# Performance work log

Hardware: AMD Instinct MI355X
Metric: run time of the kernel (lower is better)

The kernel has to match this reference:

```python
import jax, jax.numpy as jnp
import numpy as np

B, S, D = 4, 2048, 1024
H = 16
HD = D // H  # 64

def setup_inputs() -> dict:
    key = jax.random.key(0)
    ks = jax.random.split(key, 7)
    s = 0.02
    return {
        "x": jax.random.normal(ks[0], (B, S, D), dtype=jnp.float32),
        "Wq": jax.random.normal(ks[1], (D, D), dtype=jnp.float32) * s,
        "bq": jax.random.normal(ks[2], (D,), dtype=jnp.float32) * s,
        "Wk": jax.random.normal(ks[3], (D, D), dtype=jnp.float32) * s,
        "bk": jax.random.normal(ks[4], (D,), dtype=jnp.float32) * s,
        "Wv": jax.random.normal(ks[5], (D, D), dtype=jnp.float32) * s,
        "bv": jax.random.normal(ks[6], (D,), dtype=jnp.float32) * s,
    }

def reference(x, Wq, bq, Wk, bk, Wv, bv):
    bs, seq, _ = x.shape
    q = (x @ Wq.T + bq).reshape(bs, seq, H, HD).transpose(0, 2, 1, 3)  # [b,h,s,d]
    k = (x @ Wk.T + bk).reshape(bs, seq, H, HD).transpose(0, 2, 1, 3)
    v = (x @ Wv.T + bv).reshape(bs, seq, H, HD).transpose(0, 2, 1, 3)
    scores = jnp.einsum('bhqd,bhkd->bhqk', q, k) / jnp.sqrt(jnp.float32(HD))
    probs = jax.nn.softmax(scores, axis=-1)  # dropout p=0 -> identity
    att = jnp.einsum('bhqk,bhkd->bhqd', probs, v)
    return att.transpose(0, 2, 1, 3).reshape(bs, seq, H * HD)
```

## Files before the change

kernel.cpp:

```cpp
#include <hip/hip_runtime.h>

typedef __bf16 bf16x8 __attribute__((ext_vector_type(8)));
typedef float f32x4 __attribute__((ext_vector_type(4)));
typedef float f32x16 __attribute__((ext_vector_type(16)));

#define BATCH 4
#define SEQ   2048
#define DIM   1024
#define NH    16
#define HD    64
#define ECF   0.18033688f

__device__ __forceinline__ unsigned short f2bf(float f) {
  union { float f; unsigned u; } v; v.f = f;
  unsigned u = v.u;
  u += 0x7FFF + ((u >> 16) & 1);
  return (unsigned short)(u >> 16);
}

__device__ __forceinline__ void g2lds16(const unsigned short* g, unsigned short* l) {
  __builtin_amdgcn_global_load_lds(
      (const __attribute__((address_space(1))) unsigned int*)g,
      (__attribute__((address_space(3))) unsigned int*)l, 16, 0, 0);
}

__device__ __forceinline__ unsigned packbf(float a, float b) {
  __bf16 lo = (__bf16)a, hi = (__bf16)b;
  unsigned short ul = __builtin_bit_cast(unsigned short, lo);
  unsigned short uh = __builtin_bit_cast(unsigned short, hi);
  return (unsigned)ul | ((unsigned)uh << 16);
}

__global__ __launch_bounds__(256) void cast_all_kernel(
    const float* __restrict__ x,  const float* __restrict__ Wq,
    const float* __restrict__ Wk, const float* __restrict__ Wv,
    unsigned short* __restrict__ xb,  unsigned short* __restrict__ wqb,
    unsigned short* __restrict__ wkb, unsigned short* __restrict__ wvb) {
  const int XG = (BATCH * SEQ * DIM) / 8;
  const int WG = (DIM * DIM) / 8;
  int i = blockIdx.x * 256 + threadIdx.x;
  const float* in; unsigned short* out; float sc = 1.0f; int off;
  if (i < XG)               { in = x;  out = xb;  off = i; }
  else if (i < XG + WG)     { in = Wq; out = wqb; off = i - XG; sc = ECF; }
  else if (i < XG + 2 * WG) { in = Wk; out = wkb; off = i - XG - WG; }
  else                      { in = Wv; out = wvb; off = i - XG - 2 * WG; }
  const float4* p = (const float4*)in + (size_t)off * 2;
  float4 a = p[0], b = p[1];
  unsigned short r[8];
  r[0] = f2bf(a.x * sc); r[1] = f2bf(a.y * sc); r[2] = f2bf(a.z * sc); r[3] = f2bf(a.w * sc);
  r[4] = f2bf(b.x * sc); r[5] = f2bf(b.y * sc); r[6] = f2bf(b.z * sc); r[7] = f2bf(b.w * sc);
  *(uint4*)&out[(size_t)off * 8] = *(uint4*)r;
}

__global__ __launch_bounds__(256) void gemm_qkv(
    const unsigned short* __restrict__ A,
    const unsigned short* __restrict__ Wqp, const unsigned short* __restrict__ Wkp,
    const unsigned short* __restrict__ Wvp,
    const float* __restrict__ bqp, const float* __restrict__ bkp,
    const float* __restrict__ bvp,
    unsigned short* __restrict__ oq, unsigned short* __restrict__ ok,
    unsigned short* __restrict__ ov) {
  __shared__ unsigned short As[128 * 32];
  __shared__ unsigned short Bs[128 * 32];
  const int z = blockIdx.z;
  const unsigned short* W = (z == 0) ? Wqp : (z == 1) ? Wkp : Wvp;
  const float* bias        = (z == 0) ? bqp : (z == 1) ? bkp : bvp;
  unsigned short* outp     = (z == 0) ? oq  : (z == 1) ? ok  : ov;
  const float bsc          = (z == 0) ? ECF : 1.0f;
  const int mode = (z == 2) ? 1 : 0;

  const int tid  = threadIdx.x;
  const int wave = tid >> 6;
  const int lane = tid & 63;
  const int lm   = lane & 15;
  const int qd   = lane >> 4;
  const int m0 = blockIdx.x * 128;
  const int n0 = blockIdx.y * 128;
  const int wm = (wave >> 1) * 64;
  const int wn = (wave & 1) * 64;

  const f32x4 zero = {0.f, 0.f, 0.f, 0.f};
  f32x4 acc[4][4];
#pragma unroll
  for (int i = 0; i < 4; ++i)
#pragma unroll
    for (int j = 0; j < 4; ++j) acc[i][j] = zero;

  const int srow = tid >> 2;
  const int scol = (((tid & 3) ^ ((tid >> 3) & 3))) * 8;
  const int cs   = (qd ^ ((lm >> 1) & 3)) * 8;

  for (int kt = 0; kt < DIM; kt += 32) {
    __syncthreads();
    g2lds16(&A[(size_t)(m0 + srow) * DIM + kt + scol],       &As[(size_t)tid * 8]);
    g2lds16(&A[(size_t)(m0 + 64 + srow) * DIM + kt + scol],  &As[2048 + (size_t)tid * 8]);
    g2lds16(&W[(size_t)(n0 + srow) * DIM + kt + scol],       &Bs[(size_t)tid * 8]);
    g2lds16(&W[(size_t)(n0 + 64 + srow) * DIM + kt + scol],  &Bs[2048 + (size_t)tid * 8]);
    __syncthreads();

    bf16x8 af[4], bfr[4];
#pragma unroll
    for (int i = 0; i < 4; ++i) af[i]  = *(const bf16x8*)&As[(wm + i * 16 + lm) * 32 + cs];
#pragma unroll
    for (int j = 0; j < 4; ++j) bfr[j] = *(const bf16x8*)&Bs[(wn + j * 16 + lm) * 32 + cs];
#pragma unroll
    for (int i = 0; i < 4; ++i)
#pragma unroll
      for (int j = 0; j < 4; ++j)
        acc[i][j] = __builtin_amdgcn_mfma_f32_16x16x32_bf16(af[i], bfr[j], acc[i][j], 0, 0, 0);
  }

#pragma unroll
  for (int j = 0; j < 4; ++j) {
    int col = n0 + wn + j * 16 + lm;
    float bb = bias[col] * bsc;
    int h = col >> 6, hd = col & 63;
#pragma unroll
    for (int i = 0; i < 4; ++i) {
      int rowb = m0 + wm + i * 16 + qd * 4;
      int b = rowb >> 11, s = rowb & 2047;
      if (mode == 0) {
#pragma unroll
        for (int r = 0; r < 4; ++r) {
          float v = acc[i][j][r] + bb;
          outp[((size_t)(b * NH + h) * SEQ + (s + r)) * HD + hd] = f2bf(v);
        }
      } else {
        unsigned short pk[4];
#pragma unroll
        for (int r = 0; r < 4; ++r) pk[r] = f2bf(acc[i][j][r] + bb);
        size_t idx = ((size_t)(b * NH + h) * HD + hd) * SEQ + s;
        *(uint2*)&outp[idx] = *(uint2*)pk;
      }
    }
  }
}

__global__ __launch_bounds__(256, 2) void flash_kernel(
    const unsigned short* __restrict__ Qp, const unsigned short* __restrict__ Kp,
    const unsigned short* __restrict__ Vp, float* __restrict__ out) {
  __shared__ __align__(16) unsigned short Ks[2][64 * 64];
  __shared__ __align__(16) unsigned short Vs[2][64 * 64];
  __shared__ float Ls[4][2][32];

  const int tid  = threadIdx.x;
  const int w    = tid >> 6;
  const int wpar = w & 1;
  const int lane = tid & 63;
  const int l31  = lane & 31;
  const int hi   = lane >> 5;
  const int bh   = blockIdx.y;
  const int wq0  = blockIdx.x * 256 + w * 64;

  const unsigned short* Qb = Qp + (size_t)bh * (SEQ * HD);
  const unsigned short* Kb = Kp + (size_t)bh * (SEQ * HD);
  const unsigned short* Vb = Vp + (size_t)bh * (HD * SEQ);

  bf16x8 qf[2][4];
#pragma unroll
  for (int qb = 0; qb < 2; ++qb)
#pragma unroll
    for (int db = 0; db < 4; ++db)
      qf[qb][db] = *(const bf16x8*)&Qb[(size_t)(wq0 + qb * 32 + l31) * HD + db * 16 + hi * 8];

  f32x16 o[2][2];
#pragma unroll
  for (int qb = 0; qb < 2; ++qb)
#pragma unroll
    for (int jn = 0; jn < 2; ++jn)
#pragma unroll
      for (int r = 0; r < 16; ++r) o[qb][jn][r] = 0.f;
  float psum[2] = {0.f, 0.f};

  const int c0 = tid, c1 = tid + 256;
  const int kr0 = c0 >> 3, kp0 = ((c0 & 7) ^ (kr0 & 7)) * 8;
  const int kr1 = c1 >> 3, kp1 = ((c1 & 7) ^ (kr1 & 7)) * 8;
  const int r7 = l31 & 7;

  auto STAGE = [&](int buf, int k0) {
    g2lds16(&Kb[(size_t)(k0 + kr0) * HD + kp0], &Ks[buf][c0 * 8]);
    g2lds16(&Kb[(size_t)(k0 + kr1) * HD + kp1], &Ks[buf][c1 * 8]);
    g2lds16(&Vb[(size_t)kr0 * SEQ + k0 + kp0],  &Vs[buf][c0 * 8]);
    g2lds16(&Vb[(size_t)kr1 * SEQ + k0 + kp1],  &Vs[buf][c1 * 8]);
  };

  STAGE(0, 0);
  int cur = 0;
  for (int kt = 0; kt < SEQ / 64; ++kt) {
    __syncthreads();
    if (kt + 1 < SEQ / 64) STAGE(cur ^ 1, (kt + 1) * 64);

    const unsigned short* Kc = &Ks[cur][0];
    const unsigned short* Vc = &Vs[cur][0];

    const int kbA = wpar;
    const int kbB = wpar ^ 1;

    f32x16 sA0 = {0,0,0,0,0,0,0,0,0,0,0,0,0,0,0,0};
    f32x16 sA1 = {0,0,0,0,0,0,0,0,0,0,0,0,0,0,0,0};
    f32x16 sB0 = {0,0,0,0,0,0,0,0,0,0,0,0,0,0,0,0};
    f32x16 sB1 = {0,0,0,0,0,0,0,0,0,0,0,0,0,0,0,0};
    __builtin_amdgcn_s_setprio(1);
#pragma unroll
    for (int db = 0; db < 4; ++db) {
      int ch = (db * 2 + hi) ^ r7;
      bf16x8 kf = *(const bf16x8*)&Kc[((kbA * 32 + l31) * 8 + ch) * 8];
      sA0 = __builtin_amdgcn_mfma_f32_32x32x16_bf16(kf, qf[0][db], sA0, 0, 0, 0);
      sA1 = __builtin_amdgcn_mfma_f32_32x32x16_bf16(kf, qf[1][db], sA1, 0, 0, 0);
    }
    __builtin_amdgcn_s_setprio(0);
#pragma unroll
    for (int db = 0; db < 4; ++db) {
      int ch = (db * 2 + hi) ^ r7;
      bf16x8 kf = *(const bf16x8*)&Kc[((kbB * 32 + l31) * 8 + ch) * 8];
      sB0 = __builtin_amdgcn_mfma_f32_32x32x16_bf16(kf, qf[0][db], sB0, 0, 0, 0);
      sB1 = __builtin_amdgcn_mfma_f32_32x32x16_bf16(kf, qf[1][db], sB1, 0, 0, 0);
    }

    bf16x8 paA[2][2], paB[2][2];
#define EXPPACK(SQ0, SQ1, PA) do {                                            \
    _Pragma("unroll")                                                         \
    for (int qb = 0; qb < 2; ++qb) {                                          \
      const f32x16 s = qb ? (SQ1) : (SQ0);                                    \
      float p[16];                                                            \
      _Pragma("unroll")                                                       \
      for (int r = 0; r < 16; ++r) p[r] = __builtin_amdgcn_exp2f(s[r]);       \
      psum[qb] += ((p[0] + p[1]) + (p[2] + p[3])) + ((p[4] + p[5]) + (p[6] + p[7]))  \
                + ((p[8] + p[9]) + (p[10] + p[11])) + ((p[12] + p[13]) + (p[14] + p[15])); \
      unsigned w01 = packbf(p[0],  p[1]),  w23 = packbf(p[2],  p[3]);         \
      unsigned w45 = packbf(p[4],  p[5]),  w67 = packbf(p[6],  p[7]);         \
      unsigned w89 = packbf(p[8],  p[9]),  wab = packbf(p[10], p[11]);        \
      unsigned wcd = packbf(p[12], p[13]), wef = packbf(p[14], p[15]);        \
      asm volatile("v_permlane32_swap_b32 %0, %1" : "+v"(w01), "+v"(w45));    \
      asm volatile("v_permlane32_swap_b32 %0, %1" : "+v"(w23), "+v"(w67));    \
      asm volatile("v_permlane32_swap_b32 %0, %1" : "+v"(w89), "+v"(wcd));    \
      asm volatile("v_permlane32_swap_b32 %0, %1" : "+v"(wab), "+v"(wef));    \
      union { unsigned u[4]; bf16x8 v; } flo, fhi;                            \
      flo.u[0] = w01; flo.u[1] = w23; flo.u[2] = w45; flo.u[3] = w67;         \
      fhi.u[0] = w89; fhi.u[1] = wab; fhi.u[2] = wcd; fhi.u[3] = wef;         \
      (PA)[qb][0] = flo.v;                                                    \
      (PA)[qb][1] = fhi.v;                                                    \
    }                                                                         \
  } while (0)

#define PVHALF(KB, PA) do {                                                   \
    _Pragma("unroll")                                                         \
    for (int ksl = 0; ksl < 2; ++ksl) {                                       \
      int ks = (KB) * 2 + ksl;                                                \
      _Pragma("unroll")                                                       \
      for (int jn = 0; jn < 2; ++jn) {                                        \
        int ch = (ks * 2 + hi) ^ r7;                                          \
        bf16x8 vf = *(const bf16x8*)&Vc[((jn * 32 + l31) * 8 + ch) * 8];      \
        o[0][jn] = __builtin_amdgcn_mfma_f32_32x32x16_bf16((PA)[0][ksl], vf, o[0][jn], 0, 0, 0); \
        o[1][jn] = __builtin_amdgcn_mfma_f32_32x32x16_bf16((PA)[1][ksl], vf, o[1][jn], 0, 0, 0); \
      }                                                                       \
    }                                                                         \
  } while (0)

    EXPPACK(sA0, sA1, paA);
    __builtin_amdgcn_s_setprio(1);
    PVHALF(kbA, paA);
    __builtin_amdgcn_s_setprio(0);
    EXPPACK(sB0, sB1, paB);
    __builtin_amdgcn_s_setprio(1);
    PVHALF(kbB, paB);
    __builtin_amdgcn_s_setprio(0);

#undef EXPPACK
#undef PVHALF
    cur ^= 1;
  }

#pragma unroll
  for (int qb = 0; qb < 2; ++qb) {
    float l = psum[qb] + __shfl_xor(psum[qb], 32);
    if (hi == 0) Ls[w][qb][l31] = 1.0f / l;
  }
  asm volatile("s_waitcnt lgkmcnt(0)" ::: "memory");

  const int b = bh >> 4, hh = bh & 15;
#pragma unroll
  for (int qb = 0; qb < 2; ++qb)
#pragma unroll
    for (int r = 0; r < 16; ++r) {
      int crow = (r & 3) + 8 * (r >> 2) + 4 * hi;
      float inv = Ls[w][qb][crow];
      int qrow = wq0 + qb * 32 + crow;
      float* po = &out[(size_t)(b * SEQ + qrow) * DIM + hh * HD + l31];
      po[0]  = o[qb][0][r] * inv;
      po[32] = o[qb][1][r] * inv;
    }
}

extern "C" void kernel_launch(void* const* d_in, const int* in_sizes, int n_in,
                              void* d_out, int out_size, void* d_ws, size_t ws_size,
                              hipStream_t stream) {
  const float* x  = (const float*)d_in[0];
  const float* Wq = (const float*)d_in[1];
  const float* bq = (const float*)d_in[2];
  const float* Wk = (const float*)d_in[3];
  const float* bk = (const float*)d_in[4];
  const float* Wv = (const float*)d_in[5];
  const float* bv = (const float*)d_in[6];
  float* out = (float*)d_out;

  unsigned short* ws = (unsigned short*)d_ws;
  const size_t XE = (size_t)BATCH * SEQ * DIM;
  const size_t WE = (size_t)DIM * DIM;
  unsigned short* xb  = ws;
  unsigned short* wqb = xb + XE;
  unsigned short* wkb = wqb + WE;
  unsigned short* wvb = wkb + WE;
  unsigned short* qb  = wvb + WE;
  unsigned short* kb  = qb + XE;
  unsigned short* vb  = kb + XE;

  const int total_groups = (int)(XE / 8 + 3 * (WE / 8));
  cast_all_kernel<<<total_groups / 256, 256, 0, stream>>>(
      x, Wq, Wk, Wv, xb, wqb, wkb, wvb);

  dim3 gg(64, 8, 3);
  gemm_qkv<<<gg, 256, 0, stream>>>(xb, wqb, wkb, wvb, bq, bk, bv, qb, kb, vb);

  dim3 fg(SEQ / 256, BATCH * NH);
  flash_kernel<<<fg, 256, 0, stream>>>(qb, kb, vb, out);
}
```

Baseline: 251.0 us.

## Triple-buffer K/V tiles and interleave staged loads with MFMA phases via barriers

Replaces the double-buffered K/V pipeline with a three-slot ring that prefetches two tiles ahead. Global-to-LDS copies are split into four pieces, each issued inside a different compute phase (QK^T halves, PV halves). Explicit s_barrier calls and vmcnt waits keep the waves in lockstep. The intent is to hide load latency and spread memory traffic across the loop. It also drops the per-wave-parity ordering of K halves, so all waves now read the same LDS rows at the same time. The costs are more LDS per block, which could limit occupancy at two blocks per CU, and many more barriers per iteration.

Measured after the change: 247.8 us. No clear change (-1.2%).

```diff
diff --git a/kernel.cpp b/kernel.cpp
--- a/kernel.cpp
+++ b/kernel.cpp
@@ -139,13 +139,12 @@
 __global__ __launch_bounds__(256, 2) void flash_kernel(
     const unsigned short* __restrict__ Qp, const unsigned short* __restrict__ Kp,
     const unsigned short* __restrict__ Vp, float* __restrict__ out) {
-  __shared__ __align__(16) unsigned short Ks[2][64 * 64];
-  __shared__ __align__(16) unsigned short Vs[2][64 * 64];
+  __shared__ __align__(16) unsigned short Ks[3][64 * 64];
+  __shared__ __align__(16) unsigned short Vs[3][64 * 64];
   __shared__ float Ls[4][2][32];
 
   const int tid  = threadIdx.x;
   const int w    = tid >> 6;
-  const int wpar = w & 1;
   const int lane = tid & 63;
   const int l31  = lane & 31;
   const int hi   = lane >> 5;
@@ -177,47 +176,12 @@
   const int kr1 = c1 >> 3, kp1 = ((c1 & 7) ^ (kr1 & 7)) * 8;
   const int r7 = l31 & 7;
 
-  auto STAGE = [&](int buf, int k0) {
-    g2lds16(&Kb[(size_t)(k0 + kr0) * HD + kp0], &Ks[buf][c0 * 8]);
-    g2lds16(&Kb[(size_t)(k0 + kr1) * HD + kp1], &Ks[buf][c1 * 8]);
-    g2lds16(&Vb[(size_t)kr0 * SEQ + k0 + kp0],  &Vs[buf][c0 * 8]);
-    g2lds16(&Vb[(size_t)kr1 * SEQ + k0 + kp1],  &Vs[buf][c1 * 8]);
-  };
-
-  STAGE(0, 0);
-  int cur = 0;
-  for (int kt = 0; kt < SEQ / 64; ++kt) {
-    __syncthreads();
-    if (kt + 1 < SEQ / 64) STAGE(cur ^ 1, (kt + 1) * 64);
-
-    const unsigned short* Kc = &Ks[cur][0];
-    const unsigned short* Vc = &Vs[cur][0];
-
-    const int kbA = wpar;
-    const int kbB = wpar ^ 1;
-
-    f32x16 sA0 = {0,0,0,0,0,0,0,0,0,0,0,0,0,0,0,0};
-    f32x16 sA1 = {0,0,0,0,0,0,0,0,0,0,0,0,0,0,0,0};
-    f32x16 sB0 = {0,0,0,0,0,0,0,0,0,0,0,0,0,0,0,0};
-    f32x16 sB1 = {0,0,0,0,0,0,0,0,0,0,0,0,0,0,0,0};
-    __builtin_amdgcn_s_setprio(1);
-#pragma unroll
-    for (int db = 0; db < 4; ++db) {
-      int ch = (db * 2 + hi) ^ r7;
-      bf16x8 kf = *(const bf16x8*)&Kc[((kbA * 32 + l31) * 8 + ch) * 8];
-      sA0 = __builtin_amdgcn_mfma_f32_32x32x16_bf16(kf, qf[0][db], sA0, 0, 0, 0);
-      sA1 = __builtin_amdgcn_mfma_f32_32x32x16_bf16(kf, qf[1][db], sA1, 0, 0, 0);
-    }
-    __builtin_amdgcn_s_setprio(0);
-#pragma unroll
-    for (int db = 0; db < 4; ++db) {
-      int ch = (db * 2 + hi) ^ r7;
-      bf16x8 kf = *(const bf16x8*)&Kc[((kbB * 32 + l31) * 8 + ch) * 8];
-      sB0 = __builtin_amdgcn_mfma_f32_32x32x16_bf16(kf, qf[0][db], sB0, 0, 0, 0);
-      sB1 = __builtin_amdgcn_mfma_f32_32x32x16_bf16(kf, qf[1][db], sB1, 0, 0, 0);
-    }
-
-    bf16x8 paA[2][2], paB[2][2];
+#define SK0(buf, k0) g2lds16(&Kb[(size_t)((k0) + kr0) * HD + kp0], &Ks[buf][c0 * 8])
+#define SK1(buf, k0) g2lds16(&Kb[(size_t)((k0) + kr1) * HD + kp1], &Ks[buf][c1 * 8])
+#define SV0(buf, k0) g2lds16(&Vb[(size_t)kr0 * SEQ + (k0) + kp0],  &Vs[buf][c0 * 8])
+#define SV1(buf, k0) g2lds16(&Vb[(size_t)kr1 * SEQ + (k0) + kp1],  &Vs[buf][c1 * 8])
+#define BAR() asm volatile("s_barrier" ::: "memory")
+
 #define EXPPACK(SQ0, SQ1, PA) do {                                            \
     _Pragma("unroll")                                                         \
     for (int qb = 0; qb < 2; ++qb) {                                          \
@@ -243,32 +207,103 @@
     }                                                                         \
   } while (0)
 
-#define PVHALF(KB, PA) do {                                                   \
-    _Pragma("unroll")                                                         \
-    for (int ksl = 0; ksl < 2; ++ksl) {                                       \
-      int ks = (KB) * 2 + ksl;                                                \
-      _Pragma("unroll")                                                       \
-      for (int jn = 0; jn < 2; ++jn) {                                        \
-        int ch = (ks * 2 + hi) ^ r7;                                          \
-        bf16x8 vf = *(const bf16x8*)&Vc[((jn * 32 + l31) * 8 + ch) * 8];      \
-        o[0][jn] = __builtin_amdgcn_mfma_f32_32x32x16_bf16((PA)[0][ksl], vf, o[0][jn], 0, 0, 0); \
-        o[1][jn] = __builtin_amdgcn_mfma_f32_32x32x16_bf16((PA)[1][ksl], vf, o[1][jn], 0, 0, 0); \
-      }                                                                       \
-    }                                                                         \
-  } while (0)
-
-    EXPPACK(sA0, sA1, paA);
-    __builtin_amdgcn_s_setprio(1);
-    PVHALF(kbA, paA);
-    __builtin_amdgcn_s_setprio(0);
-    EXPPACK(sB0, sB1, paB);
-    __builtin_amdgcn_s_setprio(1);
-    PVHALF(kbB, paB);
-    __builtin_amdgcn_s_setprio(0);
-
-#undef EXPPACK
-#undef PVHALF
-    cur ^= 1;
+  SK0(0, 0);  SK1(0, 0);  SV0(0, 0);  SV1(0, 0);
+  SK0(1, 64); SK1(1, 64); SV0(1, 64); SV1(1, 64);
+  asm volatile("s_waitcnt vmcnt(4)" ::: "memory");
+  BAR();
+
+  for (int kt = 0; kt < 32; ++kt) {
+    const int cur = kt % 3;
+    const int nb  = (kt + 2) % 3;
+    const bool st = (kt + 2) < 32;
+    const int k2  = (kt + 2) * 64;
+    const unsigned short* Kc = &Ks[cur][0];
+    const unsigned short* Vc = &Vs[cur][0];
+
+    f32x16 sA0 = {0,0,0,0,0,0,0,0,0,0,0,0,0,0,0,0};
+    f32x16 sA1 = {0,0,0,0,0,0,0,0,0,0,0,0,0,0,0,0};
+    {
+      bf16x8 kf[4];
+#pragma unroll
+      for (int db = 0; db < 4; ++db)
+        kf[db] = *(const bf16x8*)&Kc[((0 * 32 + l31) * 8 + ((db * 2 + hi) ^ r7)) * 8];
+      if (st) SK0(nb, k2);
+      BAR();
+      __builtin_amdgcn_s_setprio(1);
+#pragma unroll
+      for (int db = 0; db < 4; ++db) {
+        sA0 = __builtin_amdgcn_mfma_f32_32x32x16_bf16(kf[db], qf[0][db], sA0, 0, 0, 0);
+        sA1 = __builtin_amdgcn_mfma_f32_32x32x16_bf16(kf[db], qf[1][db], sA1, 0, 0, 0);
+      }
+      __builtin_amdgcn_s_setprio(0);
+      BAR();
+    }
+
+    f32x16 sB0 = {0,0,0,0,0,0,0,0,0,0,0,0,0,0,0,0};
+    f32x16 sB1 = {0,0,0,0,0,0,0,0,0,0,0,0,0,0,0,0};
+    bf16x8 paA[2][2], paB[2][2];
+    {
+      bf16x8 kf[4];
+#pragma unroll
+      for (int db = 0; db < 4; ++db)
+        kf[db] = *(const bf16x8*)&Kc[((1 * 32 + l31) * 8 + ((db * 2 + hi) ^ r7)) * 8];
+      if (st) SK1(nb, k2);
+      EXPPACK(sA0, sA1, paA);
+      BAR();
+      __builtin_amdgcn_s_setprio(1);
+#pragma unroll
+      for (int db = 0; db < 4; ++db) {
+        sB0 = __builtin_amdgcn_mfma_f32_32x32x16_bf16(kf[db], qf[0][db], sB0, 0, 0, 0);
+        sB1 = __builtin_amdgcn_mfma_f32_32x32x16_bf16(kf[db], qf[1][db], sB1, 0, 0, 0);
+      }
+      __builtin_amdgcn_s_setprio(0);
+      BAR();
+    }
+
+    {
+      bf16x8 vf[2][2];
+#pragma unroll
+      for (int ksl = 0; ksl < 2; ++ksl)
+#pragma unroll
+        for (int jn = 0; jn < 2; ++jn)
+          vf[ksl][jn] = *(const bf16x8*)&Vc[((jn * 32 + l31) * 8 + ((ksl * 2 + hi) ^ r7)) * 8];
+      if (st) SV0(nb, k2);
+      EXPPACK(sB0, sB1, paB);
+      BAR();
+      __builtin_amdgcn_s_setprio(1);
+#pragma unroll
+      for (int ksl = 0; ksl < 2; ++ksl)
+#pragma unroll
+        for (int jn = 0; jn < 2; ++jn) {
+          o[0][jn] = __builtin_amdgcn_mfma_f32_32x32x16_bf16(paA[0][ksl], vf[ksl][jn], o[0][jn], 0, 0, 0);
+          o[1][jn] = __builtin_amdgcn_mfma_f32_32x32x16_bf16(paA[1][ksl], vf[ksl][jn], o[1][jn], 0, 0, 0);
+        }
+      __builtin_amdgcn_s_setprio(0);
+      BAR();
+    }
+
+    {
+      bf16x8 vf[2][2];
+#pragma unroll
+      for (int ksl = 0; ksl < 2; ++ksl)
+#pragma unroll
+        for (int jn = 0; jn < 2; ++jn)
+          vf[ksl][jn] = *(const bf16x8*)&Vc[((jn * 32 + l31) * 8 + (((2 + ksl) * 2 + hi) ^ r7)) * 8];
+      if (st) SV1(nb, k2);
+      BAR();
+      __builtin_amdgcn_s_setprio(1);
+#pragma unroll
+      for (int ksl = 0; ksl < 2; ++ksl)
+#pragma unroll
+        for (int jn = 0; jn < 2; ++jn) {
+          o[0][jn] = __builtin_amdgcn_mfma_f32_32x32x16_bf16(paB[0][ksl], vf[ksl][jn], o[0][jn], 0, 0, 0);
+          o[1][jn] = __builtin_amdgcn_mfma_f32_32x32x16_bf16(paB[1][ksl], vf[ksl][jn], o[1][jn], 0, 0, 0);
+        }
+      __builtin_amdgcn_s_setprio(0);
+      if (st) asm volatile("s_waitcnt vmcnt(4)" ::: "memory");
+      else    asm volatile("s_waitcnt vmcnt(0)" ::: "memory");
+      BAR();
+    }
   }
 
 #pragma unroll
@@ -290,6 +325,12 @@
       po[0]  = o[qb][0][r] * inv;
       po[32] = o[qb][1][r] * inv;
     }
+#undef SK0
+#undef SK1
+#undef SV0
+#undef SV1
+#undef BAR
+#undef EXPPACK
 }
 
 extern "C" void kernel_launch(void* const* d_in, const int* in_sizes, int n_in,
```
